# Kernel tuning notes

Hardware: AMD Instinct MI355X
Metric: run time of the kernel (lower is better)

The kernel has to match this reference:

```python
import jax, jax.numpy as jnp
import numpy as np

D_MODEL, D_STATE, EXPAND = 1024, 128, 2
E = D_MODEL * EXPAND          # 2048
N = D_STATE                   # 128
H = 1
P = E
TD = D_STATE // 2             # 64
Z_DIM = E + E + N + N + H + H + TD + H  # 4369
EPS = 1e-05
B_SZ, L = 4, 2048


def setup_inputs() -> dict:
    key = jax.random.key(0)
    ks = jax.random.split(key, 6)
    u = jax.random.normal(ks[0], (B_SZ, L, D_MODEL), dtype=jnp.float32)
    W_in = jax.random.normal(ks[1], (Z_DIM, D_MODEL), dtype=jnp.float32) * 0.02
    W_out = jax.random.normal(ks[2], (D_MODEL, E), dtype=jnp.float32) * 0.02
    w_normB = jnp.ones((N,), jnp.float32)
    w_normC = jnp.ones((N,), jnp.float32)
    B_bias = jnp.ones((N,), jnp.float32)
    C_bias = jnp.ones((N,), jnp.float32)
    # dt_bias buffer: dt_i ~ logU(0.001, 0.1); dt_bias = dt_i + log(-expm1(-dt_i))
    dt_i = jnp.exp(jax.random.uniform(ks[3], (H,)) * (np.log(0.1) - np.log(0.001)) + np.log(0.001))
    dt_i = jnp.clip(dt_i, 1e-4, None)
    dt_bias = dt_i + jnp.log(-jnp.expm1(-dt_i))
    A_log = jnp.full((H,), np.log(0.5), jnp.float32)
    return {"u": u, "W_in": W_in, "w_normB": w_normB, "w_normC": w_normC,
            "B_bias": B_bias, "C_bias": C_bias, "dt_bias": dt_bias,
            "A_log": A_log, "W_out": W_out}


def _rms(x, w):
    return x * jax.lax.rsqrt(jnp.mean(x * x, axis=-1, keepdims=True) + EPS) * w


def _rope(x, ang):
    half = x.shape[-1] // 2
    x1, x2 = x[..., :half], x[..., half:]
    c, s = jnp.cos(ang), jnp.sin(ang)
    return jnp.concatenate([x1 * c - x2 * s, x1 * s + x2 * c], axis=-1)


def reference(u, W_in, w_normB, w_normC, B_bias, C_bias, dt_bias, A_log, W_out):
    Bb, Ls, _ = u.shape
    z = u @ W_in.T  # [B, L, Z_DIM]
    o = 0
    def take(n):
        nonlocal o
        r = z[..., o:o + n]; o += n; return r
    x = jax.nn.silu(take(E))
    gate = jax.nn.silu(take(E))
    B_ = take(N)
    C_ = take(N)
    dt_ = take(H)
    A_ = take(H)
    th = take(TD)
    lam_ = take(H)

    dt = jax.nn.softplus(dt_ + dt_bias)          # [B, L, H]
    A = -jax.nn.softplus(A_ + A_log)             # [B, L, H]
    lam = jax.nn.sigmoid(lam_)                   # [B, L, H]
    alpha = jnp.exp(dt * A)                      # [B, L, H]

    B_ = _rms(B_, w_normB) + B_bias
    C_ = _rms(C_, w_normC) + C_bias
    ca = jnp.cumsum(jnp.mean(dt, axis=-1, keepdims=True) * th, axis=1)  # [B, L, TD]
    B_ = _rope(B_, ca)
    C_ = _rope(C_, ca)

    xh = x.reshape(Bb, Ls, H, P)
    xp = jnp.concatenate([jnp.zeros_like(xh[:, :1]), xh[:, :-1]], axis=1)  # roll + zero t=0
    lh = lam[..., None]
    xt = lh * xh + (1.0 - lh) * alpha[..., None] * xp  # [B, L, H, P]

    # fallback SSM: per-channel mean drive, per-head scalar A (mean over batch+time)
    u_mean = jnp.mean(xt, axis=-1)               # [B, L, H]
    A_bar = jnp.mean(A, axis=(0, 1))             # [H]
    dA = jnp.exp(dt * A_bar)                     # [B, L, H]
    dBu = dt[..., None] * B_[:, :, None, :] * u_mean[..., None]  # [B, L, H, N]

    def step(state, xs):
        dA_t, dBu_t, C_t = xs                    # [B,H], [B,H,N], [B,N]
        state = dA_t[..., None] * state + dBu_t  # [B, H, N]
        y_t = jnp.einsum('bhn,bn->bh', state, C_t)
        return state, y_t

    state0 = jnp.zeros((Bb, H, N), dtype=xt.dtype)
    _, ys = jax.lax.scan(step, state0,
                         (jnp.moveaxis(dA, 1, 0), jnp.moveaxis(dBu, 1, 0), jnp.moveaxis(C_, 1, 0)))
    outs = jnp.moveaxis(ys, 0, 1)                # [B, L, H]
    y = jnp.broadcast_to(outs, (Bb, Ls, E))      # H=1 expanded to E
    return (y * gate) @ W_out.T
```

## Files before the change

kernel.cpp:

```cpp
#include <hip/hip_runtime.h>
#include <cstdint>
#include <cstddef>

typedef __bf16 bf16_t;
typedef bf16_t bf16x8 __attribute__((ext_vector_type(8)));
typedef bf16_t bf16x4 __attribute__((ext_vector_type(4)));
typedef float f32x4 __attribute__((ext_vector_type(4)));

#define B_SZ    4
#define LSEQ    2048
#define DMODEL  1024
#define EDIM    2048
#define ZDIM    4419
#define ZPAD    4608
#define ROWS    (B_SZ*LSEQ)
#define EPSV    1e-5f

#define LDU     1088
#define LDG     2112

#define SCHUNK  128
#define SCLEN   (LSEQ/SCHUNK)
#define RCH     128
#define RCLEN   (LSEQ/RCH)

__device__ __forceinline__ float softplus_f(float x){
  return fmaxf(x, 0.f) + log1pf(expf(-fabsf(x)));
}
__device__ __forceinline__ float sigmoid_f(float x){ return 1.f/(1.f+expf(-x)); }
__device__ __forceinline__ float silu_f(float x){ return x/(1.f+expf(-x)); }

__device__ __forceinline__ void gload_lds16(const void* g, void* l){
  __builtin_amdgcn_global_load_lds(
      (const __attribute__((address_space(1))) void*)g,
      (__attribute__((address_space(3))) void*)l, 16, 0, 0);
}

__device__ __forceinline__ float blockReduce128(float v, float* red, int t){
  red[t] = v; __syncthreads();
  #pragma unroll
  for (int off = 64; off > 0; off >>= 1){
    if (t < off) red[t] += red[t+off];
    __syncthreads();
  }
  float r = red[0];
  __syncthreads();
  return r;
}

__global__ __launch_bounds__(256) void prep_kernel(
    const float4* __restrict__ u4, const float4* __restrict__ win4,
    const float4* __restrict__ wout4,
    bf16_t* __restrict__ ubf, bf16_t* __restrict__ winbf, bf16_t* __restrict__ woutbf,
    float* __restrict__ Asum, float* __restrict__ xraw)
{
  size_t i = (size_t)blockIdx.x*256 + threadIdx.x;
  if (i == 0) Asum[0] = 0.f;
  if (i < ROWS) xraw[i] = 0.f;
  const size_t NU4 = (size_t)ROWS*DMODEL/4;
  const size_t NW4 = (size_t)ZPAD*DMODEL/4;
  const size_t NO4 = (size_t)DMODEL*EDIM/4;
  if (i < NU4){
    float4 v = u4[i];
    size_t e = i*4, row = e>>10, col = e&1023;
    bf16x4 o = { (bf16_t)v.x, (bf16_t)v.y, (bf16_t)v.z, (bf16_t)v.w };
    *(bf16x4*)&ubf[row*LDU + col] = o;
    return;
  }
  i -= NU4;
  if (i < NW4){
    size_t e = i*4, row = e>>10, col = e&1023;
    bf16x4 o;
    if (row < (size_t)ZDIM){
      float4 v = win4[i];
      o = bf16x4{ (bf16_t)v.x, (bf16_t)v.y, (bf16_t)v.z, (bf16_t)v.w };
    } else {
      o = bf16x4{ (bf16_t)0.f, (bf16_t)0.f, (bf16_t)0.f, (bf16_t)0.f };
    }
    *(bf16x4*)&winbf[row*LDU + col] = o;
    return;
  }
  i -= NW4;
  if (i < NO4){
    float4 v = wout4[i];
    size_t e = i*4, row = e>>11, col = e&2047;
    bf16x4 o = { (bf16_t)v.x, (bf16_t)v.y, (bf16_t)v.z, (bf16_t)v.w };
    *(bf16x4*)&woutbf[row*LDG + col] = o;
  }
}

template<int BM, int BN, int WM, int WN, int NT, int NXT, int MODE>
__global__ __launch_bounds__(512, 2) void gemmQ_kernel(
    const bf16_t* __restrict__ A, const int lda,
    const bf16_t* __restrict__ W, const int ldw,
    float* __restrict__ xraw, bf16_t* __restrict__ o_g, float* __restrict__ o_z,
    const float* __restrict__ scale, float* __restrict__ o_f)
{
  constexpr int MR = BM/WM/16;
  constexpr int NR = BN/WN/16;
  constexpr int LA = BM/64;
  constexpr int LB = BN/64;
  constexpr int BUFE = (BM+BN)*64;
  __shared__ __align__(16) bf16_t lds[BUFE*2];

  const int tid = threadIdx.x;
  const int wid = tid>>6, lane = tid&63;
  const int wr = wid / WN, wc = wid % WN;
  const int lr = lane&15;

  const int nwg = NXT*(ROWS/BM);
  const int id = blockIdx.x;
  const int rid = (id & 7)*(nwg>>3) + (id>>3);
  const int bx = rid % NXT, by = rid / NXT;
  const int m0 = by*BM, n0 = bx*BN;

  f32x4 acc[MR][NR] = {};

  auto stageA = [&](int buf, int t){
    bf16_t* lA = lds + buf*BUFE;
    const int k0 = t*64;
    #pragma unroll
    for (int q = 0; q < LA; ++q){
      int cidx = q*512 + tid;
      int row = cidx>>3, sc = (cidx&7) ^ (row&7);
      gload_lds16(A + (size_t)(m0+row)*lda + k0 + sc*8,
                  lA + (size_t)(q*512 + wid*64)*8);
    }
  };
  auto stageB = [&](int buf, int t){
    bf16_t* lB = lds + buf*BUFE + BM*64;
    const int k0 = t*64;
    #pragma unroll
    for (int q = 0; q < LB; ++q){
      int cidx = q*512 + tid;
      int row = cidx>>3, sc = (cidx&7) ^ (row&7);
      gload_lds16(W + (size_t)(n0+row)*ldw + k0 + sc*8,
                  lB + (size_t)(q*512 + wid*64)*8);
    }
  };
  auto phase = [&](int buf, int kk){
    const bf16_t* lA = lds + buf*BUFE;
    const bf16_t* lB = lA + BM*64;
    const int g = kk*4 + (lane>>4);
    bf16x8 af[MR], bfr[NR];
    #pragma unroll
    for (int n = 0; n < NR; ++n){
      int rr = wc*(BN/WN) + n*16 + lr;
      bfr[n] = *(const bf16x8*)&lB[rr*64 + ((g^(rr&7))<<3)];
    }
    #pragma unroll
    for (int m = 0; m < MR; ++m){
      int rr = wr*(BM/WM) + m*16 + lr;
      af[m] = *(const bf16x8*)&lA[rr*64 + ((g^(rr&7))<<3)];
    }
    asm volatile("s_waitcnt lgkmcnt(0)" ::: "memory");
    __builtin_amdgcn_sched_barrier(0);
    __builtin_amdgcn_s_setprio(1);
    #pragma unroll
    for (int m = 0; m < MR; ++m)
      #pragma unroll
      for (int n = 0; n < NR; ++n)
        acc[m][n] = __builtin_amdgcn_mfma_f32_16x16x32_bf16(af[m], bfr[n], acc[m][n], 0,0,0);
    __builtin_amdgcn_s_setprio(0);
  };

  stageA(0, 0); stageB(0, 0);
  int cur = 0;
  for (int t = 0; t < NT; ++t){
    const bool pf = (t+1 < NT);
    if (pf){
      stageA(cur^1, t+1);
      asm volatile("s_waitcnt vmcnt(4)" ::: "memory");
    } else {
      asm volatile("s_waitcnt vmcnt(0)" ::: "memory");
    }
    asm volatile("s_barrier" ::: "memory");
    phase(cur, 0);
    if (pf) stageB(cur^1, t+1);
    phase(cur, 1);
    asm volatile("s_barrier" ::: "memory");
    cur ^= 1;
  }

  if (MODE == 0 && n0 < 2048){
    #pragma unroll
    for (int m = 0; m < MR; ++m){
      #pragma unroll
      for (int i = 0; i < 4; ++i){
        float p = 0.f;
        #pragma unroll
        for (int n = 0; n < NR; ++n) p += silu_f(acc[m][n][i]);
        #pragma unroll
        for (int off = 8; off > 0; off >>= 1) p += __shfl_xor(p, off);
        if (lr == 0){
          int r = m0 + wr*(BM/WM) + m*16 + ((lane>>4)<<2) + i;
          atomicAdd(xraw + r, p);
        }
      }
    }
  } else {
    #pragma unroll
    for (int m = 0; m < MR; ++m){
      int rowb = m0 + wr*(BM/WM) + m*16 + ((lane>>4)<<2);
      #pragma unroll
      for (int n = 0; n < NR; ++n){
        int col = n0 + wc*(BN/WN) + n*16 + lr;
        #pragma unroll
        for (int i = 0; i < 4; ++i){
          int r = rowb + i;
          float v = acc[m][n][i];
          if (MODE == 0){
            if (col < 4096)      o_g[(size_t)r*LDG + (col-2048)] = (bf16_t)silu_f(v);
            else if (col < 4480) o_z[(size_t)r*384 + (col-4096)] = v;
          } else {
            o_f[(size_t)r*DMODEL + col] = v * scale[r];
          }
        }
      }
    }
  }
}

__global__ __launch_bounds__(128) void fuse_kernel(
    const float* __restrict__ xraw, const float* __restrict__ zs,
    const float* __restrict__ wnB, const float* __restrict__ wnC,
    const float* __restrict__ Bb, const float* __restrict__ Cb,
    const float* __restrict__ dtb, const float* __restrict__ Alog,
    float* __restrict__ Bn, float* __restrict__ Cn, float* __restrict__ dtth,
    float* __restrict__ dts, float* __restrict__ alphas, float* __restrict__ lams,
    float* __restrict__ xbar, float* Asum)
{
  __shared__ float red[128];
  int r = blockIdx.x, t = threadIdx.x;
  const float* zr = zs + (size_t)r*384;
  float bv = zr[t], cv = zr[128+t];
  float b2 = blockReduce128(bv*bv, red, t);
  float c2 = blockReduce128(cv*cv, red, t);
  float rb = rsqrtf(b2*(1.f/128.f) + EPSV);
  float rc = rsqrtf(c2*(1.f/128.f) + EPSV);
  Bn[(size_t)r*128 + t] = bv*rb*wnB[t] + Bb[t];
  Cn[(size_t)r*128 + t] = cv*rc*wnC[t] + Cb[t];

  float dt = softplus_f(zr[256] + dtb[0]);
  if (t < 64) dtth[(size_t)r*64 + t] = dt * zr[258+t];
  if (t == 0){
    float Av  = -softplus_f(zr[257] + Alog[0]);
    float lam = sigmoid_f(zr[322]);
    dts[r]    = dt;
    alphas[r] = expf(dt*Av);
    lams[r]   = lam;
    xbar[r]   = xraw[r] * (1.f/2048.f);
    atomicAdd(Asum, Av);
  }
}

__global__ __launch_bounds__(64) void rope_sum_kernel(
    const float* __restrict__ dtth, float* __restrict__ csum)
{
  int b  = blockIdx.x >> 7;
  int ch = blockIdx.x & 127;
  int d  = threadIdx.x;
  const float* base = dtth + ((size_t)b*LSEQ + (size_t)ch*RCLEN)*64 + d;
  float s = 0.f;
  #pragma unroll
  for (int i = 0; i < RCLEN; ++i) s += base[(size_t)i*64];
  csum[((size_t)b*RCH + ch)*64 + d] = s;
}

__global__ __launch_bounds__(64) void rope_prefix_kernel(float* __restrict__ csum)
{
  int b = blockIdx.x, d = threadIdx.x;
  float s = 0.f;
  for (int c = 0; c < RCH; ++c){
    size_t idx = ((size_t)b*RCH + c)*64 + d;
    float v = csum[idx]; csum[idx] = s; s += v;
  }
}

__global__ __launch_bounds__(64) void rope_apply_kernel(
    const float* __restrict__ dtth, const float* __restrict__ csum,
    float* __restrict__ Bn, float* __restrict__ Cn)
{
  int b  = blockIdx.x >> 7;
  int ch = blockIdx.x & 127;
  int d  = threadIdx.x;
  float ca = csum[((size_t)b*RCH + ch)*64 + d];
  int l0 = ch*RCLEN;
  const float* base = dtth + ((size_t)b*LSEQ)*64 + d;
  for (int l = l0; l < l0 + RCLEN; ++l){
    ca += base[(size_t)l*64];
    float sn, cs;
    sincosf(ca, &sn, &cs);
    size_t ro = ((size_t)b*LSEQ + l)*128;
    float b1 = Bn[ro+d], b2v = Bn[ro+64+d];
    Bn[ro+d]    = b1*cs - b2v*sn;
    Bn[ro+64+d] = b1*sn + b2v*cs;
    float c1 = Cn[ro+d], c2v = Cn[ro+64+d];
    Cn[ro+d]    = c1*cs - c2v*sn;
    Cn[ro+64+d] = c1*sn + c2v*cs;
  }
}

__global__ __launch_bounds__(64) void scan_local_kernel(
    const float* __restrict__ dts, const float* __restrict__ alphas,
    const float* __restrict__ lams, const float* __restrict__ xbar,
    const float* __restrict__ Asum,
    const float* __restrict__ Bn, const float* __restrict__ Cn,
    float* __restrict__ ylocal, float* __restrict__ Pfix,
    float* __restrict__ Sfin, float* __restrict__ Dch)
{
  int b  = blockIdx.x / SCHUNK;
  int ch = blockIdx.x % SCHUNK;
  int n  = threadIdx.x;
  float Abar = Asum[0] * (1.f/(float)ROWS);
  float s1 = 0.f, s2 = 0.f, P = 1.f;
  int l0 = ch*SCLEN;
  #pragma unroll
  for (int i = 0; i < SCLEN; ++i){
    int l = l0 + i;
    size_t r = (size_t)b*LSEQ + l;
    float dt = dts[r], lam = lams[r], al = alphas[r], xb = xbar[r];
    float xp = (l > 0) ? xbar[r-1] : 0.f;
    float um = lam*xb + (1.f-lam)*al*xp;
    float dA = expf(dt*Abar);
    float coef = dt*um;
    size_t ro = r*128;
    s1 = dA*s1 + coef*Bn[ro+n];
    s2 = dA*s2 + coef*Bn[ro+64+n];
    P *= dA;
    float p = s1*Cn[ro+n] + s2*Cn[ro+64+n];
    #pragma unroll
    for (int off = 32; off > 0; off >>= 1) p += __shfl_down(p, off);
    if (n == 0){ ylocal[r] = p; Pfix[r] = P; }
  }
  size_t so = ((size_t)b*SCHUNK + ch)*128;
  Sfin[so + n]      = s1;
  Sfin[so + 64 + n] = s2;
  if (n == 0) Dch[b*SCHUNK + ch] = P;
}

__global__ __launch_bounds__(128) void scan_carry_kernel(
    const float* __restrict__ Sfin, const float* __restrict__ Dch,
    float* __restrict__ Sin)
{
  int b = blockIdx.x;
  int n = threadIdx.x;
  float s = 0.f;
  for (int c = 0; c < SCHUNK; ++c){
    size_t so = ((size_t)b*SCHUNK + c)*128;
    Sin[so + n] = s;
    s = Dch[b*SCHUNK + c]*s + Sfin[so + n];
  }
}

__global__ __launch_bounds__(256) void scan_fix_kernel(
    const float* __restrict__ Cn, const float* __restrict__ Sin,
    const float* __restrict__ ylocal, const float* __restrict__ Pfix,
    float* __restrict__ outsv)
{
  int r = blockIdx.x*4 + (threadIdx.x>>6);
  int n = threadIdx.x & 63;
  int b  = r / LSEQ;
  int ch = (r % LSEQ) / SCLEN;
  const float* si = Sin + ((size_t)b*SCHUNK + ch)*128;
  size_t ro = (size_t)r*128;
  float p = Cn[ro+n]*si[n] + Cn[ro+64+n]*si[64+n];
  #pragma unroll
  for (int off = 32; off > 0; off >>= 1) p += __shfl_down(p, off);
  if (n == 0) outsv[r] = ylocal[r] + Pfix[r]*p;
}

extern "C" void kernel_launch(void* const* d_in, const int* in_sizes, int n_in,
                              void* d_out, int out_size, void* d_ws, size_t ws_size,
                              hipStream_t stream)
{
  const float* u    = (const float*)d_in[0];
  const float* W_in = (const float*)d_in[1];
  const float* wnB  = (const float*)d_in[2];
  const float* wnC  = (const float*)d_in[3];
  const float* Bb   = (const float*)d_in[4];
  const float* Cb   = (const float*)d_in[5];
  const float* dtb  = (const float*)d_in[6];
  const float* Alog = (const float*)d_in[7];
  const float* Wout = (const float*)d_in[8];
  float* out = (float*)d_out;
  char* ws = (char*)d_ws;

  constexpr size_t OFF_ASUM = 0;
  constexpr size_t OFF_UBF  = 256;
  constexpr size_t SZ_UBF   = (size_t)ROWS*LDU*2;
  constexpr size_t OFF_WIN  = OFF_UBF + SZ_UBF;
  constexpr size_t SZ_WIN   = (size_t)ZPAD*LDU*2;
  constexpr size_t OFF_WOUT = OFF_WIN + SZ_WIN;
  constexpr size_t SZ_WOUT  = (size_t)DMODEL*LDG*2;
  constexpr size_t OFF_G    = OFF_WOUT + SZ_WOUT;
  constexpr size_t SZ_G     = (size_t)ROWS*LDG*2;
  constexpr size_t OFF_ZS   = OFF_G + SZ_G;
  constexpr size_t SZ_ZS    = (size_t)ROWS*384*4;
  constexpr size_t OFF_BN   = OFF_ZS + SZ_ZS;
  constexpr size_t SZ_BN    = (size_t)ROWS*128*4;
  constexpr size_t OFF_CN   = OFF_BN + SZ_BN;
  constexpr size_t OFF_DTTH = OFF_CN + SZ_BN;
  constexpr size_t SZ_DTTH  = (size_t)ROWS*64*4;
  constexpr size_t OFF_XRAW = OFF_DTTH + SZ_DTTH;
  constexpr size_t OFF_DT   = OFF_XRAW + (size_t)ROWS*4;
  constexpr size_t OFF_AL   = OFF_DT  + (size_t)ROWS*4;
  constexpr size_t OFF_LAM  = OFF_AL  + (size_t)ROWS*4;
  constexpr size_t OFF_XB   = OFF_LAM + (size_t)ROWS*4;
  constexpr size_t OFF_OUTS = OFF_XB  + (size_t)ROWS*4;
  constexpr size_t OFF_YLOC = OFF_OUTS + (size_t)ROWS*4;
  constexpr size_t OFF_PFIX = OFF_YLOC + (size_t)ROWS*4;
  constexpr size_t OFF_SFIN = OFF_PFIX + (size_t)ROWS*4;
  constexpr size_t SZ_SFIN  = (size_t)B_SZ*SCHUNK*128*4;
  constexpr size_t OFF_DCH  = OFF_SFIN + SZ_SFIN;
  constexpr size_t OFF_SIN  = OFF_DCH + (size_t)B_SZ*SCHUNK*4;
  constexpr size_t OFF_CSUM = OFF_SIN + SZ_SFIN;

  float*  Asum   = (float*) (ws + OFF_ASUM);
  bf16_t* ubf    = (bf16_t*)(ws + OFF_UBF);
  bf16_t* winbf  = (bf16_t*)(ws + OFF_WIN);
  bf16_t* woutbf = (bf16_t*)(ws + OFF_WOUT);
  bf16_t* gbuf   = (bf16_t*)(ws + OFF_G);
  float*  zsb    = (float*) (ws + OFF_ZS);
  float*  Bn     = (float*) (ws + OFF_BN);
  float*  Cn     = (float*) (ws + OFF_CN);
  float*  dtth   = (float*) (ws + OFF_DTTH);
  float*  xraw   = (float*) (ws + OFF_XRAW);
  float*  dts    = (float*) (ws + OFF_DT);
  float*  alphas = (float*) (ws + OFF_AL);
  float*  lams   = (float*) (ws + OFF_LAM);
  float*  xbar   = (float*) (ws + OFF_XB);
  float*  outsv  = (float*) (ws + OFF_OUTS);
  float*  ylocal = (float*) (ws + OFF_YLOC);
  float*  Pfix   = (float*) (ws + OFF_PFIX);
  float*  Sfin   = (float*) (ws + OFF_SFIN);
  float*  Dch    = (float*) (ws + OFF_DCH);
  float*  Sin    = (float*) (ws + OFF_SIN);
  float*  csum   = (float*) (ws + OFF_CSUM);

  {
    size_t total4 = ((size_t)ROWS*DMODEL + (size_t)ZPAD*DMODEL + (size_t)DMODEL*EDIM)/4;
    int blocks = (int)((total4 + 255)/256);
    prep_kernel<<<blocks, 256, 0, stream>>>(
        (const float4*)u, (const float4*)W_in, (const float4*)Wout,
        ubf, winbf, woutbf, Asum, xraw);
  }
  gemmQ_kernel<256, 256, 2, 4, DMODEL/64, ZPAD/256, 0>
      <<<(ZPAD/256)*(ROWS/256), 512, 0, stream>>>(
      ubf, LDU, winbf, LDU, xraw, gbuf, zsb, nullptr, nullptr);
  fuse_kernel<<<ROWS, 128, 0, stream>>>(xraw, zsb, wnB, wnC, Bb, Cb, dtb, Alog,
                                        Bn, Cn, dtth, dts, alphas, lams, xbar, Asum);
  rope_sum_kernel<<<B_SZ*RCH, 64, 0, stream>>>(dtth, csum);
  rope_prefix_kernel<<<B_SZ, 64, 0, stream>>>(csum);
  rope_apply_kernel<<<B_SZ*RCH, 64, 0, stream>>>(dtth, csum, Bn, Cn);
  scan_local_kernel<<<B_SZ*SCHUNK, 64, 0, stream>>>(dts, alphas, lams, xbar, Asum,
                                                    Bn, Cn, ylocal, Pfix, Sfin, Dch);
  scan_carry_kernel<<<B_SZ, 128, 0, stream>>>(Sfin, Dch, Sin);
  scan_fix_kernel<<<ROWS/4, 256, 0, stream>>>(Cn, Sin, ylocal, Pfix, outsv);
  gemmQ_kernel<256, 128, 4, 2, EDIM/64, DMODEL/128, 1>
      <<<(DMODEL/128)*(ROWS/256), 512, 0, stream>>>(
      gbuf, LDG, woutbf, LDG, nullptr, nullptr, nullptr, outsv, out);
}
```

Measured before the change: 323.0 us.

## Switch GEMMs to 128x256 tiles with triple-buffered LDS prefetch

Both GEMMs now use one fixed 128x256 tile with 8 waves in a 2x4 layout and a 3-stage LDS ring. Global loads for k-step t+2 are issued while k-step t computes, and LDS fragment reads are split out of the MFMA phase. The goal is to hide global-load latency better and even out tile counts across the two GEMMs. The cost is more LDS per block (144KB with 3 buffers), which may cap occupancy below the 2 blocks per CU requested, plus extra barriers per k-step.

```diff
diff --git a/kernel.cpp b/kernel.cpp
--- a/kernel.cpp
+++ b/kernel.cpp
@@ -89,23 +89,21 @@
   }
 }
 
-template<int BM, int BN, int WM, int WN, int NT, int NXT, int MODE>
-__global__ __launch_bounds__(512, 2) void gemmQ_kernel(
+template<int NT, int NXT, int MODE>
+__global__ __launch_bounds__(512, 2) void gemm8P_kernel(
     const bf16_t* __restrict__ A, const int lda,
     const bf16_t* __restrict__ W, const int ldw,
     float* __restrict__ xraw, bf16_t* __restrict__ o_g, float* __restrict__ o_z,
     const float* __restrict__ scale, float* __restrict__ o_f)
 {
-  constexpr int MR = BM/WM/16;
-  constexpr int NR = BN/WN/16;
-  constexpr int LA = BM/64;
-  constexpr int LB = BN/64;
+  constexpr int BM = 128, BN = 256;
+  constexpr int MR = 4, NR = 4;
   constexpr int BUFE = (BM+BN)*64;
-  __shared__ __align__(16) bf16_t lds[BUFE*2];
+  __shared__ __align__(16) bf16_t lds[BUFE*3];
 
   const int tid = threadIdx.x;
   const int wid = tid>>6, lane = tid&63;
-  const int wr = wid / WN, wc = wid % WN;
+  const int wr = wid>>2, wc = wid&3;
   const int lr = lane&15;
 
   const int nwg = NXT*(ROWS/BM);
@@ -120,7 +118,7 @@
     bf16_t* lA = lds + buf*BUFE;
     const int k0 = t*64;
     #pragma unroll
-    for (int q = 0; q < LA; ++q){
+    for (int q = 0; q < BM/64; ++q){
       int cidx = q*512 + tid;
       int row = cidx>>3, sc = (cidx&7) ^ (row&7);
       gload_lds16(A + (size_t)(m0+row)*lda + k0 + sc*8,
@@ -131,55 +129,76 @@
     bf16_t* lB = lds + buf*BUFE + BM*64;
     const int k0 = t*64;
     #pragma unroll
-    for (int q = 0; q < LB; ++q){
+    for (int q = 0; q < BN/64; ++q){
       int cidx = q*512 + tid;
       int row = cidx>>3, sc = (cidx&7) ^ (row&7);
       gload_lds16(W + (size_t)(n0+row)*ldw + k0 + sc*8,
                   lB + (size_t)(q*512 + wid*64)*8);
     }
   };
-  auto phase = [&](int buf, int kk){
+  auto dsread = [&](int buf, int kk, bf16x8* af, bf16x8* bfr){
     const bf16_t* lA = lds + buf*BUFE;
     const bf16_t* lB = lA + BM*64;
     const int g = kk*4 + (lane>>4);
-    bf16x8 af[MR], bfr[NR];
     #pragma unroll
     for (int n = 0; n < NR; ++n){
-      int rr = wc*(BN/WN) + n*16 + lr;
+      int rr = wc*64 + n*16 + lr;
       bfr[n] = *(const bf16x8*)&lB[rr*64 + ((g^(rr&7))<<3)];
     }
     #pragma unroll
     for (int m = 0; m < MR; ++m){
-      int rr = wr*(BM/WM) + m*16 + lr;
+      int rr = wr*64 + m*16 + lr;
       af[m] = *(const bf16x8*)&lA[rr*64 + ((g^(rr&7))<<3)];
     }
-    asm volatile("s_waitcnt lgkmcnt(0)" ::: "memory");
-    __builtin_amdgcn_sched_barrier(0);
-    __builtin_amdgcn_s_setprio(1);
-    #pragma unroll
-    for (int m = 0; m < MR; ++m)
-      #pragma unroll
-      for (int n = 0; n < NR; ++n)
-        acc[m][n] = __builtin_amdgcn_mfma_f32_16x16x32_bf16(af[m], bfr[n], acc[m][n], 0,0,0);
-    __builtin_amdgcn_s_setprio(0);
   };
 
   stageA(0, 0); stageB(0, 0);
+  stageA(1, 1); stageB(1, 1);
+  asm volatile("s_waitcnt vmcnt(6)" ::: "memory");
+  __builtin_amdgcn_s_barrier();
+
   int cur = 0;
   for (int t = 0; t < NT; ++t){
-    const bool pf = (t+1 < NT);
-    if (pf){
-      stageA(cur^1, t+1);
-      asm volatile("s_waitcnt vmcnt(4)" ::: "memory");
-    } else {
-      asm volatile("s_waitcnt vmcnt(0)" ::: "memory");
-    }
-    asm volatile("s_barrier" ::: "memory");
-    phase(cur, 0);
-    if (pf) stageB(cur^1, t+1);
-    phase(cur, 1);
-    asm volatile("s_barrier" ::: "memory");
-    cur ^= 1;
+    int nb = cur + 2; if (nb >= 3) nb -= 3;
+    const bool pf = (t+2 < NT);
+    {
+      bf16x8 af[MR], bfr[NR];
+      dsread(cur, 0, af, bfr);
+      if (pf) stageA(nb, t+2);
+      __builtin_amdgcn_s_barrier();
+      asm volatile("s_waitcnt lgkmcnt(0)" ::: "memory");
+      __builtin_amdgcn_sched_barrier(0);
+      __builtin_amdgcn_s_setprio(1);
+      #pragma unroll
+      for (int m = 0; m < MR; ++m)
+        #pragma unroll
+        for (int n = 0; n < NR; ++n)
+          acc[m][n] = __builtin_amdgcn_mfma_f32_16x16x32_bf16(af[m], bfr[n], acc[m][n], 0,0,0);
+      __builtin_amdgcn_s_setprio(0);
+      __builtin_amdgcn_s_barrier();
+    }
+    {
+      bf16x8 af[MR], bfr[NR];
+      dsread(cur, 1, af, bfr);
+      if (pf){
+        stageB(nb, t+2);
+        asm volatile("s_waitcnt vmcnt(6)" ::: "memory");
+      } else {
+        asm volatile("s_waitcnt vmcnt(0)" ::: "memory");
+      }
+      __builtin_amdgcn_s_barrier();
+      asm volatile("s_waitcnt lgkmcnt(0)" ::: "memory");
+      __builtin_amdgcn_sched_barrier(0);
+      __builtin_amdgcn_s_setprio(1);
+      #pragma unroll
+      for (int m = 0; m < MR; ++m)
+        #pragma unroll
+        for (int n = 0; n < NR; ++n)
+          acc[m][n] = __builtin_amdgcn_mfma_f32_16x16x32_bf16(af[m], bfr[n], acc[m][n], 0,0,0);
+      __builtin_amdgcn_s_setprio(0);
+      __builtin_amdgcn_s_barrier();
+    }
+    if (++cur == 3) cur = 0;
   }
 
   if (MODE == 0 && n0 < 2048){
@@ -193,7 +212,7 @@
         #pragma unroll
         for (int off = 8; off > 0; off >>= 1) p += __shfl_xor(p, off);
         if (lr == 0){
-          int r = m0 + wr*(BM/WM) + m*16 + ((lane>>4)<<2) + i;
+          int r = m0 + wr*64 + m*16 + ((lane>>4)<<2) + i;
           atomicAdd(xraw + r, p);
         }
       }
@@ -201,10 +220,10 @@
   } else {
     #pragma unroll
     for (int m = 0; m < MR; ++m){
-      int rowb = m0 + wr*(BM/WM) + m*16 + ((lane>>4)<<2);
+      int rowb = m0 + wr*64 + m*16 + ((lane>>4)<<2);
       #pragma unroll
       for (int n = 0; n < NR; ++n){
-        int col = n0 + wc*(BN/WN) + n*16 + lr;
+        int col = n0 + wc*64 + n*16 + lr;
         #pragma unroll
         for (int i = 0; i < 4; ++i){
           int r = rowb + i;
@@ -445,8 +464,8 @@
         (const float4*)u, (const float4*)W_in, (const float4*)Wout,
         ubf, winbf, woutbf, Asum, xraw);
   }
-  gemmQ_kernel<256, 256, 2, 4, DMODEL/64, ZPAD/256, 0>
-      <<<(ZPAD/256)*(ROWS/256), 512, 0, stream>>>(
+  gemm8P_kernel<DMODEL/64, ZPAD/256, 0>
+      <<<(ZPAD/256)*(ROWS/128), 512, 0, stream>>>(
       ubf, LDU, winbf, LDU, xraw, gbuf, zsb, nullptr, nullptr);
   fuse_kernel<<<ROWS, 128, 0, stream>>>(xraw, zsb, wnB, wnC, Bb, Cb, dtb, Alog,
                                         Bn, Cn, dtth, dts, alphas, lams, xbar, Asum);
@@ -457,7 +476,7 @@
                                                     Bn, Cn, ylocal, Pfix, Sfin, Dch);
   scan_carry_kernel<<<B_SZ, 128, 0, stream>>>(Sfin, Dch, Sin);
   scan_fix_kernel<<<ROWS/4, 256, 0, stream>>>(Cn, Sin, ylocal, Pfix, outsv);
-  gemmQ_kernel<256, 128, 4, 2, EDIM/64, DMODEL/128, 1>
-      <<<(DMODEL/128)*(ROWS/256), 512, 0, stream>>>(
+  gemm8P_kernel<EDIM/64, DMODEL/256, 1>
+      <<<(DMODEL/256)*(ROWS/128), 512, 0, stream>>>(
       gbuf, LDG, woutbf, LDG, nullptr, nullptr, nullptr, outsv, out);
 }
```

Measured after the change: 330.3 us. 2.2% more time.

## Rewrite GEMMs with finer-grained load/MFMA interleaving and split-K output GEMM

Applied to the files above, without the earlier changes.

Replaces the templated GEMM with a fixed 256x256-tile kernel that interleaves half-tile async global-to-LDS loads with alternating LDS reads and MFMA groups, separated by explicit barriers. Loads are issued through precomputed pointers that advance each step. The output projection now uses 256-wide tiles and a two-way split-K, with atomic float adds into an output buffer zeroed by a new memset. This aims to hide memory latency better and fill the GPU during the second GEMM, at the cost of more barriers, atomic traffic and an extra memset.

```diff
diff --git a/kernel.cpp b/kernel.cpp
--- a/kernel.cpp
+++ b/kernel.cpp
@@ -89,132 +89,179 @@
   }
 }
 
-template<int BM, int BN, int WM, int WN, int NT, int NXT, int MODE>
-__global__ __launch_bounds__(512, 2) void gemmQ_kernel(
-    const bf16_t* __restrict__ A, const int lda,
-    const bf16_t* __restrict__ W, const int ldw,
+template<int LDA_, int LDW_, int NT, int NXT, int MODE>
+__global__ __launch_bounds__(512, 2) void gemmHK_kernel(
+    const bf16_t* __restrict__ A0, const bf16_t* __restrict__ W0,
     float* __restrict__ xraw, bf16_t* __restrict__ o_g, float* __restrict__ o_z,
     const float* __restrict__ scale, float* __restrict__ o_f)
 {
-  constexpr int MR = BM/WM/16;
-  constexpr int NR = BN/WN/16;
-  constexpr int LA = BM/64;
-  constexpr int LB = BN/64;
-  constexpr int BUFE = (BM+BN)*64;
-  __shared__ __align__(16) bf16_t lds[BUFE*2];
+  constexpr int BUF1 = 32768;
+  __shared__ __align__(16) bf16_t lds[BUF1*2];
 
   const int tid = threadIdx.x;
   const int wid = tid>>6, lane = tid&63;
-  const int wr = wid / WN, wc = wid % WN;
-  const int lr = lane&15;
-
-  const int nwg = NXT*(ROWS/BM);
+  const int wr = wid>>2, wc = wid&3;
+  const int lr = lane&15, hi = lane>>4, lr7 = lane&7;
+
+  constexpr int NWG = (MODE==0) ? NXT*(ROWS/256) : NXT*(ROWS/256)*2;
   const int id = blockIdx.x;
-  const int rid = (id & 7)*(nwg>>3) + (id>>3);
-  const int bx = rid % NXT, by = rid / NXT;
-  const int m0 = by*BM, n0 = bx*BN;
-
-  f32x4 acc[MR][NR] = {};
-
-  auto stageA = [&](int buf, int t){
-    bf16_t* lA = lds + buf*BUFE;
-    const int k0 = t*64;
+  const int rid = (id & 7)*(NWG/8) + (id>>3);
+  int bx, by, kz = 0;
+  if (MODE == 0){ bx = rid % NXT; by = rid / NXT; }
+  else { kz = rid / (NXT*(ROWS/256)); int r2 = rid % (NXT*(ROWS/256));
+         bx = r2 % NXT; by = r2 / NXT; }
+  const int m0 = by*256, n0 = bx*256;
+  const bf16_t* A = A0 + (size_t)kz*1024;
+  const bf16_t* W = W0 + (size_t)kz*1024;
+
+  f32x4 acc[8][4] = {};
+  bf16x8 af[4], bfr[4];
+
+  const bf16_t* pA[4]; const bf16_t* pB[4];
+  bf16_t* dA[4]; bf16_t* dB[4];
+  #pragma unroll
+  for (int q = 0; q < 4; ++q){
+    int cidx = q*512 + tid;
+    int row = cidx>>3, sc = (cidx&7) ^ (row&7);
+    pA[q] = A + (size_t)(m0+row)*LDA_ + sc*8;
+    pB[q] = W + (size_t)(n0+row)*LDW_ + sc*8;
+    dA[q] = &lds[(q*512 + wid*64)*8];
+    dB[q] = &lds[16384 + (q*512 + wid*64)*8];
+  }
+
+  auto stage_lo = [&](int bo) __attribute__((always_inline)) {
+    gload_lds16(pA[0], dA[0]+bo); pA[0] += 64;
+    gload_lds16(pA[1], dA[1]+bo); pA[1] += 64;
+    gload_lds16(pB[0], dB[0]+bo); pB[0] += 64;
+    gload_lds16(pB[1], dB[1]+bo); pB[1] += 64;
+  };
+  auto stage_hi = [&](int bo) __attribute__((always_inline)) {
+    gload_lds16(pA[2], dA[2]+bo); pA[2] += 64;
+    gload_lds16(pA[3], dA[3]+bo); pA[3] += 64;
+    gload_lds16(pB[2], dB[2]+bo); pB[2] += 64;
+    gload_lds16(pB[3], dB[3]+bo); pB[3] += 64;
+  };
+  auto dsread = [&](int bo, int mh, int ks, bool readB) __attribute__((always_inline)) {
+    const int g = ks*4 + hi;
+    const int swz = (g ^ lr7) << 3;
+    if (readB){
+      const int bb = bo + 16384 + ((wc*64 + lr)<<6) + swz;
+      #pragma unroll
+      for (int n = 0; n < 4; ++n)
+        bfr[n] = *(const bf16x8*)&lds[bb + n*1024];
+    }
+    const int ab = bo + ((wr*16 + lr)<<6) + swz + mh*8192;
     #pragma unroll
-    for (int q = 0; q < LA; ++q){
-      int cidx = q*512 + tid;
-      int row = cidx>>3, sc = (cidx&7) ^ (row&7);
-      gload_lds16(A + (size_t)(m0+row)*lda + k0 + sc*8,
-                  lA + (size_t)(q*512 + wid*64)*8);
-    }
+    for (int m = 0; m < 4; ++m)
+      af[m] = *(const bf16x8*)&lds[ab + m*2048];
   };
-  auto stageB = [&](int buf, int t){
-    bf16_t* lB = lds + buf*BUFE + BM*64;
-    const int k0 = t*64;
-    #pragma unroll
-    for (int q = 0; q < LB; ++q){
-      int cidx = q*512 + tid;
-      int row = cidx>>3, sc = (cidx&7) ^ (row&7);
-      gload_lds16(W + (size_t)(n0+row)*ldw + k0 + sc*8,
-                  lB + (size_t)(q*512 + wid*64)*8);
-    }
-  };
-  auto phase = [&](int buf, int kk){
-    const bf16_t* lA = lds + buf*BUFE;
-    const bf16_t* lB = lA + BM*64;
-    const int g = kk*4 + (lane>>4);
-    bf16x8 af[MR], bfr[NR];
-    #pragma unroll
-    for (int n = 0; n < NR; ++n){
-      int rr = wc*(BN/WN) + n*16 + lr;
-      bfr[n] = *(const bf16x8*)&lB[rr*64 + ((g^(rr&7))<<3)];
-    }
-    #pragma unroll
-    for (int m = 0; m < MR; ++m){
-      int rr = wr*(BM/WM) + m*16 + lr;
-      af[m] = *(const bf16x8*)&lA[rr*64 + ((g^(rr&7))<<3)];
-    }
+  auto domfma = [&](int mh) __attribute__((always_inline)) {
     asm volatile("s_waitcnt lgkmcnt(0)" ::: "memory");
     __builtin_amdgcn_sched_barrier(0);
     __builtin_amdgcn_s_setprio(1);
     #pragma unroll
-    for (int m = 0; m < MR; ++m)
+    for (int m = 0; m < 4; ++m)
       #pragma unroll
-      for (int n = 0; n < NR; ++n)
-        acc[m][n] = __builtin_amdgcn_mfma_f32_16x16x32_bf16(af[m], bfr[n], acc[m][n], 0,0,0);
+      for (int n = 0; n < 4; ++n)
+        acc[mh*4+m][n] = __builtin_amdgcn_mfma_f32_16x16x32_bf16(af[m], bfr[n], acc[mh*4+m][n], 0,0,0);
     __builtin_amdgcn_s_setprio(0);
   };
 
-  stageA(0, 0); stageB(0, 0);
-  int cur = 0;
-  for (int t = 0; t < NT; ++t){
-    const bool pf = (t+1 < NT);
-    if (pf){
-      stageA(cur^1, t+1);
-      asm volatile("s_waitcnt vmcnt(4)" ::: "memory");
-    } else {
-      asm volatile("s_waitcnt vmcnt(0)" ::: "memory");
-    }
-    asm volatile("s_barrier" ::: "memory");
-    phase(cur, 0);
-    if (pf) stageB(cur^1, t+1);
-    phase(cur, 1);
-    asm volatile("s_barrier" ::: "memory");
-    cur ^= 1;
-  }
+  stage_lo(0); stage_hi(0); stage_lo(BUF1);
+  asm volatile("s_waitcnt vmcnt(4)" ::: "memory");
+  __builtin_amdgcn_s_barrier();
+
+  auto iter = [&](bool full) __attribute__((always_inline)) {
+    dsread(0, 0, 0, true); stage_hi(BUF1);
+    __builtin_amdgcn_s_barrier();
+    domfma(0);
+    __builtin_amdgcn_s_barrier();
+    dsread(0, 1, 0, false);
+    __builtin_amdgcn_s_barrier();
+    domfma(1);
+    __builtin_amdgcn_s_barrier();
+    dsread(0, 0, 1, true);
+    __builtin_amdgcn_s_barrier();
+    domfma(0);
+    __builtin_amdgcn_s_barrier();
+    dsread(0, 1, 1, false);
+    if (full) stage_lo(0);
+    __builtin_amdgcn_s_barrier();
+    domfma(1);
+    if (full) { asm volatile("s_waitcnt vmcnt(4)" ::: "memory"); }
+    else      { asm volatile("s_waitcnt vmcnt(0)" ::: "memory"); }
+    __builtin_amdgcn_s_barrier();
+    dsread(BUF1, 0, 0, true);
+    if (full) stage_hi(0);
+    __builtin_amdgcn_s_barrier();
+    domfma(0);
+    __builtin_amdgcn_s_barrier();
+    dsread(BUF1, 1, 0, false);
+    __builtin_amdgcn_s_barrier();
+    domfma(1);
+    __builtin_amdgcn_s_barrier();
+    dsread(BUF1, 0, 1, true);
+    __builtin_amdgcn_s_barrier();
+    domfma(0);
+    __builtin_amdgcn_s_barrier();
+    dsread(BUF1, 1, 1, false);
+    if (full) stage_lo(BUF1);
+    __builtin_amdgcn_s_barrier();
+    domfma(1);
+    if (full) { asm volatile("s_waitcnt vmcnt(4)" ::: "memory"); }
+    else      { asm volatile("s_waitcnt vmcnt(0)" ::: "memory"); }
+    __builtin_amdgcn_s_barrier();
+  };
+
+  constexpr int NI = NT/2;
+  #pragma unroll 1
+  for (int it = 0; it < NI-1; ++it) iter(true);
+  iter(false);
 
   if (MODE == 0 && n0 < 2048){
     #pragma unroll
-    for (int m = 0; m < MR; ++m){
+    for (int macc = 0; macc < 8; ++macc){
       #pragma unroll
       for (int i = 0; i < 4; ++i){
         float p = 0.f;
         #pragma unroll
-        for (int n = 0; n < NR; ++n) p += silu_f(acc[m][n][i]);
+        for (int n = 0; n < 4; ++n) p += silu_f(acc[macc][n][i]);
+        p += __shfl_xor(p, 8); p += __shfl_xor(p, 4);
+        p += __shfl_xor(p, 2); p += __shfl_xor(p, 1);
+        if (lr == 0){
+          int r = m0 + macc*32 + wr*16 + (hi<<2) + i;
+          atomicAdd(xraw + r, p);
+        }
+      }
+    }
+  } else if (MODE == 0){
+    #pragma unroll
+    for (int macc = 0; macc < 8; ++macc){
+      int rowb = m0 + macc*32 + wr*16 + (hi<<2);
+      #pragma unroll
+      for (int n = 0; n < 4; ++n){
+        int col = n0 + wc*64 + n*16 + lr;
         #pragma unroll
-        for (int off = 8; off > 0; off >>= 1) p += __shfl_xor(p, off);
-        if (lr == 0){
-          int r = m0 + wr*(BM/WM) + m*16 + ((lane>>4)<<2) + i;
-          atomicAdd(xraw + r, p);
+        for (int i = 0; i < 4; ++i){
+          int r = rowb + i;
+          float v = acc[macc][n][i];
+          if (col < 4096)      o_g[(size_t)r*LDG + (col-2048)] = (bf16_t)silu_f(v);
+          else if (col < 4480) o_z[(size_t)r*384 + (col-4096)] = v;
         }
       }
     }
   } else {
     #pragma unroll
-    for (int m = 0; m < MR; ++m){
-      int rowb = m0 + wr*(BM/WM) + m*16 + ((lane>>4)<<2);
+    for (int macc = 0; macc < 8; ++macc){
+      int rowb = m0 + macc*32 + wr*16 + (hi<<2);
       #pragma unroll
-      for (int n = 0; n < NR; ++n){
-        int col = n0 + wc*(BN/WN) + n*16 + lr;
+      for (int i = 0; i < 4; ++i){
+        int r = rowb + i;
+        float s = scale[r];
         #pragma unroll
-        for (int i = 0; i < 4; ++i){
-          int r = rowb + i;
-          float v = acc[m][n][i];
-          if (MODE == 0){
-            if (col < 4096)      o_g[(size_t)r*LDG + (col-2048)] = (bf16_t)silu_f(v);
-            else if (col < 4480) o_z[(size_t)r*384 + (col-4096)] = v;
-          } else {
-            o_f[(size_t)r*DMODEL + col] = v * scale[r];
-          }
+        for (int n = 0; n < 4; ++n){
+          int col = n0 + wc*64 + n*16 + lr;
+          atomicAdd(o_f + (size_t)r*DMODEL + col, acc[macc][n][i]*s);
         }
       }
     }
@@ -445,9 +492,11 @@
         (const float4*)u, (const float4*)W_in, (const float4*)Wout,
         ubf, winbf, woutbf, Asum, xraw);
   }
-  gemmQ_kernel<256, 256, 2, 4, DMODEL/64, ZPAD/256, 0>
+  hipMemsetAsync(out, 0, (size_t)ROWS*DMODEL*sizeof(float), stream);
+
+  gemmHK_kernel<LDU, LDU, DMODEL/64, ZPAD/256, 0>
       <<<(ZPAD/256)*(ROWS/256), 512, 0, stream>>>(
-      ubf, LDU, winbf, LDU, xraw, gbuf, zsb, nullptr, nullptr);
+      ubf, winbf, xraw, gbuf, zsb, nullptr, nullptr);
   fuse_kernel<<<ROWS, 128, 0, stream>>>(xraw, zsb, wnB, wnC, Bb, Cb, dtb, Alog,
                                         Bn, Cn, dtth, dts, alphas, lams, xbar, Asum);
   rope_sum_kernel<<<B_SZ*RCH, 64, 0, stream>>>(dtth, csum);
@@ -457,7 +506,7 @@
                                                     Bn, Cn, ylocal, Pfix, Sfin, Dch);
   scan_carry_kernel<<<B_SZ, 128, 0, stream>>>(Sfin, Dch, Sin);
   scan_fix_kernel<<<ROWS/4, 256, 0, stream>>>(Cn, Sin, ylocal, Pfix, outsv);
-  gemmQ_kernel<256, 128, 4, 2, EDIM/64, DMODEL/128, 1>
-      <<<(DMODEL/128)*(ROWS/256), 512, 0, stream>>>(
-      gbuf, LDG, woutbf, LDG, nullptr, nullptr, nullptr, outsv, out);
-}
+  gemmHK_kernel<LDG, LDG, 1024/64, DMODEL/256, 1>
+      <<<2*(DMODEL/256)*(ROWS/256), 512, 0, stream>>>(
+      gbuf, woutbf, nullptr, nullptr, nullptr, outsv, out);
+}
```

Result: slower. 369.7 us (+14.5%).

## Replace double-buffered GEMM with single-buffer 256x128 tile, 4-wave kernel

Applied to the files above, without the earlier changes.

Replaces the templated 512-thread, double-buffered GEMM with a 256-thread kernel using a fixed 256x128 tile, K-step 32, single LDS buffer and precomputed swizzled offsets. Aims for higher occupancy (3 blocks per CU) and less LDS use. The input GEMM now tiles N at 128 instead of 256. The cost is that loads are no longer overlapped with MFMA inside a block, so each iteration synchronizes twice and load latency is only hidden by running more blocks. Epilogues are specialized per mode, and the output-scale load is hoisted.

```diff
diff --git a/kernel.cpp b/kernel.cpp
--- a/kernel.cpp
+++ b/kernel.cpp
@@ -89,132 +89,126 @@
   }
 }
 
-template<int BM, int BN, int WM, int WN, int NT, int NXT, int MODE>
-__global__ __launch_bounds__(512, 2) void gemmQ_kernel(
-    const bf16_t* __restrict__ A, const int lda,
-    const bf16_t* __restrict__ W, const int ldw,
+template<int LDA_, int LDW_, int NT, int NXT, int MODE>
+__global__ __launch_bounds__(256, 3) void gemmS_kernel(
+    const bf16_t* __restrict__ A0, const bf16_t* __restrict__ W0,
     float* __restrict__ xraw, bf16_t* __restrict__ o_g, float* __restrict__ o_z,
     const float* __restrict__ scale, float* __restrict__ o_f)
 {
-  constexpr int MR = BM/WM/16;
-  constexpr int NR = BN/WN/16;
-  constexpr int LA = BM/64;
-  constexpr int LB = BN/64;
-  constexpr int BUFE = (BM+BN)*64;
-  __shared__ __align__(16) bf16_t lds[BUFE*2];
+  __shared__ __align__(16) bf16_t lds[(256+128)*32];
 
   const int tid = threadIdx.x;
   const int wid = tid>>6, lane = tid&63;
-  const int wr = wid / WN, wc = wid % WN;
-  const int lr = lane&15;
-
-  const int nwg = NXT*(ROWS/BM);
+  const int wr = wid>>1, wc = wid&1;
+  const int lr = lane&15, hi = lane>>4;
+
+  constexpr int NWG = NXT*(ROWS/256);
   const int id = blockIdx.x;
-  const int rid = (id & 7)*(nwg>>3) + (id>>3);
+  const int rid = (id & 7)*(NWG/8) + (id>>3);
   const int bx = rid % NXT, by = rid / NXT;
-  const int m0 = by*BM, n0 = bx*BN;
-
-  f32x4 acc[MR][NR] = {};
-
-  auto stageA = [&](int buf, int t){
-    bf16_t* lA = lds + buf*BUFE;
-    const int k0 = t*64;
-    #pragma unroll
-    for (int q = 0; q < LA; ++q){
-      int cidx = q*512 + tid;
-      int row = cidx>>3, sc = (cidx&7) ^ (row&7);
-      gload_lds16(A + (size_t)(m0+row)*lda + k0 + sc*8,
-                  lA + (size_t)(q*512 + wid*64)*8);
+  const int m0 = by*256, n0 = bx*128;
+
+  f32x4 acc[8][4] = {};
+
+  int gAoff[4], lAoff[4], gBoff[2], lBoff[2];
+  #pragma unroll
+  for (int q = 0; q < 4; ++q){
+    int cidx = q*256 + tid;
+    int row = cidx>>2, ch = cidx&3;
+    int sc = ch ^ (row&3) ^ ((row>>2)&3);
+    gAoff[q] = row*LDA_ + sc*8;
+    lAoff[q] = cidx*8;
+  }
+  #pragma unroll
+  for (int q = 0; q < 2; ++q){
+    int cidx = q*256 + tid;
+    int row = cidx>>2, ch = cidx&3;
+    int sc = ch ^ (row&3) ^ ((row>>2)&3);
+    gBoff[q] = row*LDW_ + sc*8;
+    lBoff[q] = 8192 + cidx*8;
+  }
+  int aoff[8], boff[4];
+  #pragma unroll
+  for (int m = 0; m < 8; ++m){
+    int row = wr*128 + m*16 + lr;
+    int sc = hi ^ (row&3) ^ ((row>>2)&3);
+    aoff[m] = row*32 + sc*8;
+  }
+  #pragma unroll
+  for (int n = 0; n < 4; ++n){
+    int row = wc*64 + n*16 + lr;
+    int sc = hi ^ (row&3) ^ ((row>>2)&3);
+    boff[n] = 8192 + row*32 + sc*8;
+  }
+
+  const bf16_t* Ak = A0 + (size_t)m0*LDA_;
+  const bf16_t* Wk = W0 + (size_t)n0*LDW_;
+
+  #pragma unroll 1
+  for (int t = 0; t < NT; ++t){
+    #pragma unroll
+    for (int q = 0; q < 4; ++q) gload_lds16(Ak + gAoff[q], &lds[lAoff[q]]);
+    #pragma unroll
+    for (int q = 0; q < 2; ++q) gload_lds16(Wk + gBoff[q], &lds[lBoff[q]]);
+    Ak += 32; Wk += 32;
+    __syncthreads();
+    bf16x8 bfr[4];
+    #pragma unroll
+    for (int n = 0; n < 4; ++n) bfr[n] = *(const bf16x8*)&lds[boff[n]];
+    #pragma unroll
+    for (int m = 0; m < 8; ++m){
+      bf16x8 af = *(const bf16x8*)&lds[aoff[m]];
+      #pragma unroll
+      for (int n = 0; n < 4; ++n)
+        acc[m][n] = __builtin_amdgcn_mfma_f32_16x16x32_bf16(af, bfr[n], acc[m][n], 0,0,0);
     }
-  };
-  auto stageB = [&](int buf, int t){
-    bf16_t* lB = lds + buf*BUFE + BM*64;
-    const int k0 = t*64;
-    #pragma unroll
-    for (int q = 0; q < LB; ++q){
-      int cidx = q*512 + tid;
-      int row = cidx>>3, sc = (cidx&7) ^ (row&7);
-      gload_lds16(W + (size_t)(n0+row)*ldw + k0 + sc*8,
-                  lB + (size_t)(q*512 + wid*64)*8);
-    }
-  };
-  auto phase = [&](int buf, int kk){
-    const bf16_t* lA = lds + buf*BUFE;
-    const bf16_t* lB = lA + BM*64;
-    const int g = kk*4 + (lane>>4);
-    bf16x8 af[MR], bfr[NR];
-    #pragma unroll
-    for (int n = 0; n < NR; ++n){
-      int rr = wc*(BN/WN) + n*16 + lr;
-      bfr[n] = *(const bf16x8*)&lB[rr*64 + ((g^(rr&7))<<3)];
-    }
-    #pragma unroll
-    for (int m = 0; m < MR; ++m){
-      int rr = wr*(BM/WM) + m*16 + lr;
-      af[m] = *(const bf16x8*)&lA[rr*64 + ((g^(rr&7))<<3)];
-    }
-    asm volatile("s_waitcnt lgkmcnt(0)" ::: "memory");
-    __builtin_amdgcn_sched_barrier(0);
-    __builtin_amdgcn_s_setprio(1);
-    #pragma unroll
-    for (int m = 0; m < MR; ++m)
-      #pragma unroll
-      for (int n = 0; n < NR; ++n)
-        acc[m][n] = __builtin_amdgcn_mfma_f32_16x16x32_bf16(af[m], bfr[n], acc[m][n], 0,0,0);
-    __builtin_amdgcn_s_setprio(0);
-  };
-
-  stageA(0, 0); stageB(0, 0);
-  int cur = 0;
-  for (int t = 0; t < NT; ++t){
-    const bool pf = (t+1 < NT);
-    if (pf){
-      stageA(cur^1, t+1);
-      asm volatile("s_waitcnt vmcnt(4)" ::: "memory");
-    } else {
-      asm volatile("s_waitcnt vmcnt(0)" ::: "memory");
-    }
-    asm volatile("s_barrier" ::: "memory");
-    phase(cur, 0);
-    if (pf) stageB(cur^1, t+1);
-    phase(cur, 1);
-    asm volatile("s_barrier" ::: "memory");
-    cur ^= 1;
+    __syncthreads();
   }
 
   if (MODE == 0 && n0 < 2048){
     #pragma unroll
-    for (int m = 0; m < MR; ++m){
+    for (int m = 0; m < 8; ++m){
       #pragma unroll
       for (int i = 0; i < 4; ++i){
         float p = 0.f;
         #pragma unroll
-        for (int n = 0; n < NR; ++n) p += silu_f(acc[m][n][i]);
-        #pragma unroll
-        for (int off = 8; off > 0; off >>= 1) p += __shfl_xor(p, off);
+        for (int n = 0; n < 4; ++n) p += silu_f(acc[m][n][i]);
+        p += __shfl_xor(p, 8); p += __shfl_xor(p, 4);
+        p += __shfl_xor(p, 2); p += __shfl_xor(p, 1);
         if (lr == 0){
-          int r = m0 + wr*(BM/WM) + m*16 + ((lane>>4)<<2) + i;
+          int r = m0 + wr*128 + m*16 + (hi<<2) + i;
           atomicAdd(xraw + r, p);
         }
       }
     }
-  } else {
-    #pragma unroll
-    for (int m = 0; m < MR; ++m){
-      int rowb = m0 + wr*(BM/WM) + m*16 + ((lane>>4)<<2);
+  } else if (MODE == 0){
+    #pragma unroll
+    for (int m = 0; m < 8; ++m){
+      int rowb = m0 + wr*128 + m*16 + (hi<<2);
       #pragma unroll
-      for (int n = 0; n < NR; ++n){
-        int col = n0 + wc*(BN/WN) + n*16 + lr;
+      for (int n = 0; n < 4; ++n){
+        int col = n0 + wc*64 + n*16 + lr;
         #pragma unroll
         for (int i = 0; i < 4; ++i){
           int r = rowb + i;
           float v = acc[m][n][i];
-          if (MODE == 0){
-            if (col < 4096)      o_g[(size_t)r*LDG + (col-2048)] = (bf16_t)silu_f(v);
-            else if (col < 4480) o_z[(size_t)r*384 + (col-4096)] = v;
-          } else {
-            o_f[(size_t)r*DMODEL + col] = v * scale[r];
-          }
+          if (col < 4096)      o_g[(size_t)r*LDG + (col-2048)] = (bf16_t)silu_f(v);
+          else if (col < 4480) o_z[(size_t)r*384 + (col-4096)] = v;
+        }
+      }
+    }
+  } else {
+    #pragma unroll
+    for (int m = 0; m < 8; ++m){
+      int rowb = m0 + wr*128 + m*16 + (hi<<2);
+      #pragma unroll
+      for (int i = 0; i < 4; ++i){
+        int r = rowb + i;
+        float s = scale[r];
+        #pragma unroll
+        for (int n = 0; n < 4; ++n){
+          int col = n0 + wc*64 + n*16 + lr;
+          o_f[(size_t)r*DMODEL + col] = acc[m][n][i]*s;
         }
       }
     }
@@ -445,9 +439,9 @@
         (const float4*)u, (const float4*)W_in, (const float4*)Wout,
         ubf, winbf, woutbf, Asum, xraw);
   }
-  gemmQ_kernel<256, 256, 2, 4, DMODEL/64, ZPAD/256, 0>
-      <<<(ZPAD/256)*(ROWS/256), 512, 0, stream>>>(
-      ubf, LDU, winbf, LDU, xraw, gbuf, zsb, nullptr, nullptr);
+  gemmS_kernel<LDU, LDU, 32, ZPAD/128, 0>
+      <<<(ZPAD/128)*(ROWS/256), 256, 0, stream>>>(
+      ubf, winbf, xraw, gbuf, zsb, nullptr, nullptr);
   fuse_kernel<<<ROWS, 128, 0, stream>>>(xraw, zsb, wnB, wnC, Bb, Cb, dtb, Alog,
                                         Bn, Cn, dtth, dts, alphas, lams, xbar, Asum);
   rope_sum_kernel<<<B_SZ*RCH, 64, 0, stream>>>(dtth, csum);
@@ -457,7 +451,7 @@
                                                     Bn, Cn, ylocal, Pfix, Sfin, Dch);
   scan_carry_kernel<<<B_SZ, 128, 0, stream>>>(Sfin, Dch, Sin);
   scan_fix_kernel<<<ROWS/4, 256, 0, stream>>>(Cn, Sin, ylocal, Pfix, outsv);
-  gemmQ_kernel<256, 128, 4, 2, EDIM/64, DMODEL/128, 1>
-      <<<(DMODEL/128)*(ROWS/256), 512, 0, stream>>>(
-      gbuf, LDG, woutbf, LDG, nullptr, nullptr, nullptr, outsv, out);
-}
+  gemmS_kernel<LDG, LDG, 64, DMODEL/128, 1>
+      <<<(DMODEL/128)*(ROWS/256), 256, 0, stream>>>(
+      gbuf, woutbf, nullptr, nullptr, nullptr, outsv, out);
+}
```

Result: slower. 353.3 us (+9.4%).
